# Kernel tuning notes

Hardware: AMD Instinct MI355X
Metric: run time of the kernel (lower is better)

The kernel has to match this reference:

```python
import jax, jax.numpy as jnp
import numpy as np

T, B, C, N, H = 4, 8, 256, 2048, 16
D = C // H          # head dim = 16
SCALE = 0.25        # fixed scale in SCA_AV
EPS = 1e-5          # BatchNorm eps


def _conv_bn(h_in, w, gamma, beta):
    """1x1 Conv1d (bias=False) + BatchNorm1d in training mode.
    h_in: [T,B,C,N]; w: [C_out,C_in]; BN stats over (T,B,N) per channel."""
    h = jnp.einsum('oc,tbcn->tbon', w, h_in)
    mean = h.mean(axis=(0, 1, 3), keepdims=True)
    var = ((h - mean) ** 2).mean(axis=(0, 1, 3), keepdims=True)
    return gamma[None, None, :, None] * (h - mean) * jax.lax.rsqrt(var + EPS) + beta[None, None, :, None]


def _spike(h, vth):
    # MyNode called once after reset: mem = 0/tau + h; spike = (mem >= vth)
    return (h >= vth).astype(h.dtype)


def _heads(z):
    # [T,B,C,N] -> [T,B,H,N,D] (channel index c = h*D + d, matching torch reshape)
    return z.reshape(T, B, H, D, N).transpose(0, 1, 2, 4, 3)


def setup_inputs() -> dict:
    key = jax.random.key(0)
    ks = jax.random.split(key, 16)
    s = 1.0 / np.sqrt(C)
    inp = {
        'x': jax.random.normal(ks[0], (T, B, C, N), jnp.float32),
        'y': jax.random.normal(ks[1], (T, B, C, N), jnp.float32),
        'q_w': jax.random.normal(ks[2], (C, C), jnp.float32) * s,
        'q_gamma': jnp.ones((C,), jnp.float32),
        'q_beta': jnp.zeros((C,), jnp.float32),
        'k_w': jax.random.normal(ks[3], (C, C), jnp.float32) * s,
        'k_gamma': jnp.ones((C,), jnp.float32),
        'k_beta': jnp.zeros((C,), jnp.float32),
        'v_w': jax.random.normal(ks[4], (C, C), jnp.float32) * s,
        'v_gamma': jnp.ones((C,), jnp.float32),
        'v_beta': jnp.zeros((C,), jnp.float32),
        'proj_w': jax.random.normal(ks[5], (C, C), jnp.float32) * s,
        'proj_gamma': jnp.ones((C,), jnp.float32),
        'proj_beta': jnp.zeros((C,), jnp.float32),
    }
    return inp


def reference(x, y, q_w, q_gamma, q_beta, k_w, k_gamma, k_beta,
              v_w, v_gamma, v_beta, proj_w, proj_gamma, proj_beta):
    # spiking Q from x, spiking K/V from y
    q = _heads(_spike(_conv_bn(x, q_w, q_gamma, q_beta), 1.0))  # [T,B,H,N,D] in {0,1}
    k = _heads(_spike(_conv_bn(y, k_w, k_gamma, k_beta), 1.0))
    v = _heads(_spike(_conv_bn(y, v_w, v_gamma, v_beta), 1.0))
    # linear-attention reordering: (q @ k^T) @ v == q @ (k^T @ v); kv is only DxD
    kv = jnp.einsum('tbhnd,tbhne->tbhde', k, v)          # [T,B,H,D,D]
    o = jnp.einsum('tbhnd,tbhde->tbhne', q, kv) * SCALE  # [T,B,H,N,D]
    # back to [T,B,C,N] (transpose(3,4) then reshape, as in torch)
    o = o.transpose(0, 1, 2, 4, 3).reshape(T, B, C, N)
    s = _spike(o, 0.5)                                   # attn_lif, v_threshold=0.5
    out = _spike(_conv_bn(s, proj_w, proj_gamma, proj_beta), 1.0)  # proj + proj_lif
    return out
```

## Files before the change

### kernel.cpp

```cpp
#include <hip/hip_runtime.h>
#include <stdint.h>
#include <math.h>

#define T_ 4
#define B_ 8
#define C_ 256
#define N_ 2048
#define TB_ 32
#define H_ 16
#define D_ 16
#define NTOT 65536
#define EPS 1e-5
#define NSLOT 1024
#define WPSZ 327680

typedef int v4i __attribute__((ext_vector_type(4)));

__global__ __launch_bounds__(256) void wprep_kernel(const float* __restrict__ W0,
                                                    const float* __restrict__ W1,
                                                    const float* __restrict__ W2,
                                                    int8_t* __restrict__ out) {
  const float* Wm = (blockIdx.y == 0) ? W0 : ((blockIdx.y == 1) ? W1 : W2);
  const int o = blockIdx.x;
  const int c = (int)threadIdx.x;
  double rr = rint((double)Wm[o * C_ + c] * 0x1p40);
  int8_t* base = out + (size_t)blockIdx.y * WPSZ + (size_t)(c >> 4) * 20480 +
                 (size_t)o * 80 + (c & 15);
#pragma unroll
  for (int L = 0; L < 5; ++L) {
    const double q = floor(fma(rr, 0.00390625, 0.5));
    const double d = fma(q, -256.0, rr);
    base[L * 16] = (int8_t)(int)d;
    rr = q;
  }
}

__global__ __launch_bounds__(256) void xprep_kernel(const float* __restrict__ X,
                                                    uint8_t* __restrict__ XP) {
  __shared__ float Xs[64][81];
  const int n0 = blockIdx.x * 64;
  const int tb = blockIdx.y;
  const int tid = (int)threadIdx.x;
  const int c_l = tid >> 2, nc = tid & 3;
  const int n_l = tid & 63, cq = tid >> 6;

  const float* Xp = X + ((size_t)(tb * C_ + c_l)) * N_ + n0 + nc * 16;

  for (int slab = 0; slab < 4; ++slab) {
    __syncthreads();
#pragma unroll
    for (int r = 0; r < 4; ++r) {
      const float4 xv = *(const float4*)(Xp + (size_t)(slab * 64) * N_ + 4 * r);
      Xs[c_l][nc * 16 + 4 * r + 0] = xv.x;
      Xs[c_l][nc * 16 + 4 * r + 1] = xv.y;
      Xs[c_l][nc * 16 + 4 * r + 2] = xv.z;
      Xs[c_l][nc * 16 + 4 * r + 3] = xv.w;
    }
    __syncthreads();
    uint32_t pk[4][4] = {};
#pragma unroll
    for (int s = 0; s < 16; ++s) {
      const float f = Xs[cq * 16 + s][n_l];
      union { double d; unsigned long long u; } cv;
      cv.d = fma((double)f, 0x1p28, 0x1.8p52);
      int v = (int)(uint32_t)(cv.u & 0xffffffffULL);
      const int d0 = (int)(int8_t)v;  v = (v - d0) >> 8;
      const int d1 = (int)(int8_t)v;  v = (v - d1) >> 8;
      const int d2 = (int)(int8_t)v;
      const int d3 = (v - d2) >> 8;
      const int sh = 8 * (s & 3);
      const int w = s >> 2;
      pk[0][w] |= (uint32_t)(d0 & 255) << sh;
      pk[1][w] |= (uint32_t)(d1 & 255) << sh;
      pk[2][w] |= (uint32_t)(d2 & 255) << sh;
      pk[3][w] |= (uint32_t)(d3 & 255) << sh;
    }
    uint8_t* dst =
        XP + (((size_t)(tb * 16 + slab * 4 + cq)) * (size_t)N_ + n0 + n_l) * 64;
#pragma unroll
    for (int j = 0; j < 4; ++j) {
      const int4 wv = make_int4((int)pk[j][0], (int)pk[j][1], (int)pk[j][2], (int)pk[j][3]);
      *(int4*)(dst + 16 * j) = wv;
    }
  }
}

template <bool QKV, bool STATS, typename OutT>
__global__ __launch_bounds__(256) void conv_i8(
    const int8_t* __restrict__ WP, const uint8_t* __restrict__ BP,
    double* __restrict__ Psum, double* __restrict__ Psq,
    const float* __restrict__ gamma, const float* __restrict__ beta,
    const double* __restrict__ mean, const double* __restrict__ invstd,
    OutT* __restrict__ Out) {
  __shared__ double dsum[4][64];
  __shared__ double dsq[4][64];
  __shared__ double aS[64];
  __shared__ double bS[64];
  const int n0 = blockIdx.x * 64;
  const int o0 = blockIdx.y * 64;
  const int tb = blockIdx.z;
  const int tid = (int)threadIdx.x;
  const int wv = tid >> 6;
  const int lane = tid & 63;
  const int l15 = lane & 15;
  const int g = lane >> 4;
  const int nn = 16 * wv + l15;

  if constexpr (!STATS) {
    if (tid < 64) {
      const int c = o0 + tid;
      const double is = invstd[c], mu = mean[c];
      const double gm = (double)gamma[c], bt = (double)beta[c];
      aS[tid] = gm * is;
      bS[tid] = bt - gm * mu * is;
    }
    __syncthreads();
  }

  v4i acc[4][5] = {};

  for (int slab = 0; slab < 4; ++slab) {
    const int cc = slab * 4 + g;
    v4i Bf[4];
    if constexpr (QKV) {
      const uint8_t* bp = BP + (((size_t)(tb * 16 + cc)) * (size_t)N_ + n0 + nn) * 64;
#pragma unroll
      for (int j = 0; j < 4; ++j) Bf[j] = *(const v4i*)(bp + 16 * j);
    } else {
      Bf[0] = *(const v4i*)(BP + ((size_t)(tb * N_ + n0 + nn)) * 256 + slab * 64 + 16 * g);
    }
#pragma unroll
    for (int mt = 0; mt < 4; ++mt) {
      const int8_t* ap = WP + (size_t)cc * 20480 + (size_t)(o0 + 16 * mt + l15) * 80;
      v4i A[5];
#pragma unroll
      for (int i = 0; i < 5; ++i) A[i] = *(const v4i*)(ap + 16 * i);
      if constexpr (QKV) {
        constexpr int PI[14] = {0, 1, 2, 3, 4, 1, 2, 3, 4, 2, 3, 4, 3, 4};
        constexpr int PJ[14] = {3, 3, 3, 3, 3, 2, 2, 2, 2, 1, 1, 1, 0, 0};
#pragma unroll
        for (int p = 0; p < 14; ++p)
          acc[mt][PI[p] + PJ[p] - 3] = __builtin_amdgcn_mfma_i32_16x16x64_i8(
              A[PI[p]], Bf[PJ[p]], acc[mt][PI[p] + PJ[p] - 3], 0, 0, 0);
      } else {
#pragma unroll
        for (int i = 0; i < 5; ++i)
          acc[mt][i] = __builtin_amdgcn_mfma_i32_16x16x64_i8(A[i], Bf[0], acc[mt][i], 0, 0, 0);
      }
    }
  }

  const double scale[5] = {QKV ? 0x1p-44 : 0x1p-40, QKV ? 0x1p-36 : 0x1p-32,
                           QKV ? 0x1p-28 : 0x1p-24, QKV ? 0x1p-20 : 0x1p-16,
                           QKV ? 0x1p-12 : 0x1p-8};

  if constexpr (STATS) {
#pragma unroll
    for (int mt = 0; mt < 4; ++mt) {
      double s[4], q[4];
#pragma unroll
      for (int r = 0; r < 4; ++r) {
        double v = 0.0;
#pragma unroll
        for (int a = 0; a < 5; ++a) v = fma(scale[a], (double)acc[mt][a][r], v);
        s[r] = v;
        q[r] = v * v;
      }
#pragma unroll
      for (int m = 1; m < 16; m <<= 1) {
#pragma unroll
        for (int r = 0; r < 4; ++r) {
          s[r] += __shfl_xor(s[r], m);
          q[r] += __shfl_xor(q[r], m);
        }
      }
      if (l15 < 4) {
        dsum[wv][16 * mt + 4 * g + l15] = s[l15];
        dsq[wv][16 * mt + 4 * g + l15] = q[l15];
      }
    }
    __syncthreads();
    if (tid < 64) {
      const double S = dsum[0][tid] + dsum[1][tid] + dsum[2][tid] + dsum[3][tid];
      const double Q = dsq[0][tid] + dsq[1][tid] + dsq[2][tid] + dsq[3][tid];
      const int slot = tb * 32 + (int)blockIdx.x;
      Psum[(size_t)(o0 + tid) * NSLOT + slot] = S;
      Psq[(size_t)(o0 + tid) * NSLOT + slot] = Q;
    }
  } else {
#pragma unroll
    for (int mt = 0; mt < 4; ++mt) {
#pragma unroll
      for (int r = 0; r < 4; ++r) {
        double v = 0.0;
#pragma unroll
        for (int a = 0; a < 5; ++a) v = fma(scale[a], (double)acc[mt][a][r], v);
        const int row = 16 * mt + 4 * g + r;
        const int sp = (aS[row] * v + bS[row] >= 1.0) ? 1 : 0;
        Out[((size_t)(tb * C_ + o0 + row)) * N_ + n0 + nn] = (OutT)sp;
      }
    }
  }
}

__global__ __launch_bounds__(256) void finalize_stats(const double* __restrict__ Psum,
                                                      const double* __restrict__ Psq,
                                                      double* __restrict__ mean,
                                                      double* __restrict__ invstd) {
  const int c = blockIdx.x;
  const int tid = (int)threadIdx.x;
  double s = 0.0, q = 0.0;
  for (int i = tid; i < NSLOT; i += 256) {
    s += Psum[(size_t)c * NSLOT + i];
    q += Psq[(size_t)c * NSLOT + i];
  }
#pragma unroll
  for (int m = 1; m < 64; m <<= 1) {
    s += __shfl_xor(s, m);
    q += __shfl_xor(q, m);
  }
  __shared__ double ls[4], lq[4];
  if ((tid & 63) == 0) {
    ls[tid >> 6] = s;
    lq[tid >> 6] = q;
  }
  __syncthreads();
  if (tid == 0) {
    const double S = ls[0] + ls[1] + ls[2] + ls[3];
    const double Q = lq[0] + lq[1] + lq[2] + lq[3];
    const double m = S / (double)NTOT;
    const double var = Q / (double)NTOT - m * m;
    mean[c] = m;
    invstd[c] = 1.0 / sqrt(var + EPS);
  }
}

__global__ __launch_bounds__(256) void attn_kernel(const uint8_t* __restrict__ Sq,
                                                   const uint8_t* __restrict__ Sk,
                                                   const uint8_t* __restrict__ Sv,
                                                   uint8_t* __restrict__ SbufT) {
  __shared__ float kvs[16][17];
  const int tb = (int)blockIdx.x >> 4;
  const int h = (int)blockIdx.x & 15;
  const size_t base = ((size_t)(tb * C_ + h * D_)) * N_;
  const int tid = (int)threadIdx.x;
  {
    const int d = tid >> 4, e = tid & 15;
    const uint32_t* kr = (const uint32_t*)(Sk + base + (size_t)d * N_);
    const uint32_t* vr = (const uint32_t*)(Sv + base + (size_t)e * N_);
    int cnt = 0;
    for (int i = 0; i < N_ / 4; ++i) cnt += __popc(kr[i] & vr[i]);
    kvs[d][e] = (float)cnt;
  }
  __syncthreads();
  for (int rep = 0; rep < 8; ++rep) {
    const int n = rep * 256 + tid;
    float qv[16];
#pragma unroll
    for (int d = 0; d < 16; ++d) qv[d] = (float)Sq[base + (size_t)d * N_ + n];
    uint32_t w[4] = {0, 0, 0, 0};
#pragma unroll
    for (int e = 0; e < 16; ++e) {
      float acc = 0.f;
#pragma unroll
      for (int d = 0; d < 16; ++d) acc += qv[d] * kvs[d][e];
      const uint32_t sp = (0.25f * acc >= 0.5f) ? 1u : 0u;
      w[e >> 2] |= sp << (8 * (e & 3));
    }
    const int4 pw = make_int4((int)w[0], (int)w[1], (int)w[2], (int)w[3]);
    *(int4*)(SbufT + ((size_t)(tb * N_ + n)) * 256 + h * 16) = pw;
  }
}

extern "C" void kernel_launch(void* const* d_in, const int* in_sizes, int n_in,
                              void* d_out, int out_size, void* d_ws, size_t ws_size,
                              hipStream_t stream) {
  const float* x   = (const float*)d_in[0];
  const float* y   = (const float*)d_in[1];
  const float* q_w = (const float*)d_in[2];
  const float* q_g = (const float*)d_in[3];
  const float* q_b = (const float*)d_in[4];
  const float* k_w = (const float*)d_in[5];
  const float* k_g = (const float*)d_in[6];
  const float* k_b = (const float*)d_in[7];
  const float* v_w = (const float*)d_in[8];
  const float* v_g = (const float*)d_in[9];
  const float* v_b = (const float*)d_in[10];
  const float* p_w = (const float*)d_in[11];
  const float* p_g = (const float*)d_in[12];
  const float* p_b = (const float*)d_in[13];
  float* out = (float*)d_out;

  char* ws = (char*)d_ws;
  const size_t NE = (size_t)TB_ * C_ * N_;
  uint8_t* XPx   = (uint8_t*)ws;
  uint8_t* XPy   = (uint8_t*)(ws + NE * 4);
  uint8_t* Sq    = (uint8_t*)(ws + NE * 8);
  uint8_t* Sk    = Sq + NE;
  uint8_t* Sv    = Sk + NE;
  uint8_t* SbufT = Sv + NE;

  double* PsumA   = (double*)SbufT;
  double* PsqA    = PsumA + (size_t)C_ * NSLOT;
  double* meanA   = PsqA + (size_t)C_ * NSLOT;
  double* invstdA = meanA + C_;
  int8_t* WPA     = (int8_t*)(SbufT + 5 * 1024 * 1024);
  int8_t* WPq     = WPA;
  int8_t* WPk     = WPA + WPSZ;
  int8_t* WPv     = WPA + 2 * WPSZ;
  double* PsumB   = (double*)Sq;
  double* PsqB    = PsumB + (size_t)C_ * NSLOT;
  double* meanB   = PsqB + (size_t)C_ * NSLOT;
  double* invstdB = meanB + C_;
  int8_t* WPB     = (int8_t*)(Sq + 8 * 1024 * 1024);

  const dim3 gridG(N_ / 64, C_ / 64, TB_);
  const dim3 blk(256);

  wprep_kernel<<<dim3(C_, 3), blk, 0, stream>>>(q_w, k_w, v_w, WPA);
  xprep_kernel<<<dim3(N_ / 64, TB_), blk, 0, stream>>>(x, XPx);
  xprep_kernel<<<dim3(N_ / 64, TB_), blk, 0, stream>>>(y, XPy);
  conv_i8<true, true, uint8_t><<<gridG, blk, 0, stream>>>(
      WPq, XPx, PsumA, PsqA, nullptr, nullptr, nullptr, nullptr, (uint8_t*)nullptr);
  finalize_stats<<<C_, blk, 0, stream>>>(PsumA, PsqA, meanA, invstdA);
  conv_i8<true, false, uint8_t><<<gridG, blk, 0, stream>>>(
      WPq, XPx, nullptr, nullptr, q_g, q_b, meanA, invstdA, Sq);
  conv_i8<true, true, uint8_t><<<gridG, blk, 0, stream>>>(
      WPk, XPy, PsumA, PsqA, nullptr, nullptr, nullptr, nullptr, (uint8_t*)nullptr);
  finalize_stats<<<C_, blk, 0, stream>>>(PsumA, PsqA, meanA, invstdA);
  conv_i8<true, false, uint8_t><<<gridG, blk, 0, stream>>>(
      WPk, XPy, nullptr, nullptr, k_g, k_b, meanA, invstdA, Sk);
  conv_i8<true, true, uint8_t><<<gridG, blk, 0, stream>>>(
      WPv, XPy, PsumA, PsqA, nullptr, nullptr, nullptr, nullptr, (uint8_t*)nullptr);
  finalize_stats<<<C_, blk, 0, stream>>>(PsumA, PsqA, meanA, invstdA);
  conv_i8<true, false, uint8_t><<<gridG, blk, 0, stream>>>(
      WPv, XPy, nullptr, nullptr, v_g, v_b, meanA, invstdA, Sv);
  attn_kernel<<<TB_ * H_, blk, 0, stream>>>(Sq, Sk, Sv, SbufT);
  wprep_kernel<<<dim3(C_, 1), blk, 0, stream>>>(p_w, p_w, p_w, WPB);
  conv_i8<false, true, float><<<gridG, blk, 0, stream>>>(
      WPB, SbufT, PsumB, PsqB, nullptr, nullptr, nullptr, nullptr, (float*)nullptr);
  finalize_stats<<<C_, blk, 0, stream>>>(PsumB, PsqB, meanB, invstdB);
  conv_i8<false, false, float><<<gridG, blk, 0, stream>>>(
      WPB, SbufT, nullptr, nullptr, p_g, p_b, meanB, invstdB, out);
}
```

Baseline: 821.9 us.

## Store conv output once and apply BN spike in separate elementwise pass

Each conv GEMM previously ran twice, once for BN statistics and once to apply BN and spike. Now it runs once, writes the pre-BN activations as a float plus an int8 residual (a split high-precision encoding) and accumulates stats, and a separate elementwise spike_pass applies the BN threshold. K and V spikes are bit-packed so the attention kv popcount reads eight times less data. The xprep buffer is reused for x and y. This trades a second MFMA GEMM for about 5 bytes per element of extra write-and-read traffic, and the residual encoding may lose precision near the threshold.

Result: faster. 677.2 us (-17.6%).

```diff
diff --git a/kernel.cpp b/kernel.cpp
--- a/kernel.cpp
+++ b/kernel.cpp
@@ -13,6 +13,7 @@
 #define EPS 1e-5
 #define NSLOT 1024
 #define WPSZ 327680
+#define MB (1024 * 1024)
 
 typedef int v4i __attribute__((ext_vector_type(4)));
 
@@ -85,17 +86,13 @@
   }
 }
 
-template <bool QKV, bool STATS, typename OutT>
-__global__ __launch_bounds__(256) void conv_i8(
+template <bool QKV>
+__global__ __launch_bounds__(256) void conv_gemm(
     const int8_t* __restrict__ WP, const uint8_t* __restrict__ BP,
-    double* __restrict__ Psum, double* __restrict__ Psq,
-    const float* __restrict__ gamma, const float* __restrict__ beta,
-    const double* __restrict__ mean, const double* __restrict__ invstd,
-    OutT* __restrict__ Out) {
+    float* __restrict__ hF, int8_t* __restrict__ hR,
+    double* __restrict__ Psum, double* __restrict__ Psq) {
   __shared__ double dsum[4][64];
   __shared__ double dsq[4][64];
-  __shared__ double aS[64];
-  __shared__ double bS[64];
   const int n0 = blockIdx.x * 64;
   const int o0 = blockIdx.y * 64;
   const int tb = blockIdx.z;
@@ -106,17 +103,6 @@
   const int g = lane >> 4;
   const int nn = 16 * wv + l15;
 
-  if constexpr (!STATS) {
-    if (tid < 64) {
-      const int c = o0 + tid;
-      const double is = invstd[c], mu = mean[c];
-      const double gm = (double)gamma[c], bt = (double)beta[c];
-      aS[tid] = gm * is;
-      bS[tid] = bt - gm * mu * is;
-    }
-    __syncthreads();
-  }
-
   v4i acc[4][5] = {};
 
   for (int slab = 0; slab < 4; ++slab) {
@@ -154,52 +140,44 @@
                            QKV ? 0x1p-28 : 0x1p-24, QKV ? 0x1p-20 : 0x1p-16,
                            QKV ? 0x1p-12 : 0x1p-8};
 
-  if constexpr (STATS) {
-#pragma unroll
-    for (int mt = 0; mt < 4; ++mt) {
-      double s[4], q[4];
+#pragma unroll
+  for (int mt = 0; mt < 4; ++mt) {
+    double s[4], q[4];
+#pragma unroll
+    for (int r = 0; r < 4; ++r) {
+      double v = 0.0;
+#pragma unroll
+      for (int a = 0; a < 5; ++a) v = fma(scale[a], (double)acc[mt][a][r], v);
+      const int row = 16 * mt + 4 * g + r;
+      const size_t idx = ((size_t)(tb * C_ + o0 + row)) * N_ + n0 + nn;
+      const float f = (float)v;
+      hF[idx] = f;
+      int ri = (int)rint((v - (double)f) * 0x1p27);
+      ri = ri < -127 ? -127 : (ri > 127 ? 127 : ri);
+      hR[idx] = (int8_t)ri;
+      s[r] = v;
+      q[r] = v * v;
+    }
+#pragma unroll
+    for (int m = 1; m < 16; m <<= 1) {
 #pragma unroll
       for (int r = 0; r < 4; ++r) {
-        double v = 0.0;
-#pragma unroll
-        for (int a = 0; a < 5; ++a) v = fma(scale[a], (double)acc[mt][a][r], v);
-        s[r] = v;
-        q[r] = v * v;
+        s[r] += __shfl_xor(s[r], m);
+        q[r] += __shfl_xor(q[r], m);
       }
-#pragma unroll
-      for (int m = 1; m < 16; m <<= 1) {
-#pragma unroll
-        for (int r = 0; r < 4; ++r) {
-          s[r] += __shfl_xor(s[r], m);
-          q[r] += __shfl_xor(q[r], m);
-        }
-      }
-      if (l15 < 4) {
-        dsum[wv][16 * mt + 4 * g + l15] = s[l15];
-        dsq[wv][16 * mt + 4 * g + l15] = q[l15];
-      }
-    }
-    __syncthreads();
-    if (tid < 64) {
-      const double S = dsum[0][tid] + dsum[1][tid] + dsum[2][tid] + dsum[3][tid];
-      const double Q = dsq[0][tid] + dsq[1][tid] + dsq[2][tid] + dsq[3][tid];
-      const int slot = tb * 32 + (int)blockIdx.x;
-      Psum[(size_t)(o0 + tid) * NSLOT + slot] = S;
-      Psq[(size_t)(o0 + tid) * NSLOT + slot] = Q;
-    }
-  } else {
-#pragma unroll
-    for (int mt = 0; mt < 4; ++mt) {
-#pragma unroll
-      for (int r = 0; r < 4; ++r) {
-        double v = 0.0;
-#pragma unroll
-        for (int a = 0; a < 5; ++a) v = fma(scale[a], (double)acc[mt][a][r], v);
-        const int row = 16 * mt + 4 * g + r;
-        const int sp = (aS[row] * v + bS[row] >= 1.0) ? 1 : 0;
-        Out[((size_t)(tb * C_ + o0 + row)) * N_ + n0 + nn] = (OutT)sp;
-      }
-    }
+    }
+    if (l15 < 4) {
+      dsum[wv][16 * mt + 4 * g + l15] = s[l15];
+      dsq[wv][16 * mt + 4 * g + l15] = q[l15];
+    }
+  }
+  __syncthreads();
+  if (tid < 64) {
+    const double S = dsum[0][tid] + dsum[1][tid] + dsum[2][tid] + dsum[3][tid];
+    const double Q = dsq[0][tid] + dsq[1][tid] + dsq[2][tid] + dsq[3][tid];
+    const int slot = tb * 32 + (int)blockIdx.x;
+    Psum[(size_t)(o0 + tid) * NSLOT + slot] = S;
+    Psq[(size_t)(o0 + tid) * NSLOT + slot] = Q;
   }
 }
 
@@ -235,21 +213,62 @@
   }
 }
 
-__global__ __launch_bounds__(256) void attn_kernel(const uint8_t* __restrict__ Sq,
-                                                   const uint8_t* __restrict__ Sk,
-                                                   const uint8_t* __restrict__ Sv,
+template <int MODE>
+__global__ __launch_bounds__(256) void spike_pass(
+    const float* __restrict__ hF, const int8_t* __restrict__ hR,
+    const float* __restrict__ gamma, const float* __restrict__ beta,
+    const double* __restrict__ mean, const double* __restrict__ invstd,
+    uint8_t* __restrict__ outB, float* __restrict__ outF) {
+  const size_t i0 = ((size_t)blockIdx.x * 256 + threadIdx.x) * 8;
+  const int c = (int)((i0 >> 11) & 255);
+  const double a = (double)gamma[c] * invstd[c];
+  const double b = (double)beta[c] - (double)gamma[c] * mean[c] * invstd[c];
+  const float4 f0 = *(const float4*)(hF + i0);
+  const float4 f1 = *(const float4*)(hF + i0 + 4);
+  const uint64_t rw = *(const uint64_t*)(hR + i0);
+  const float fs[8] = {f0.x, f0.y, f0.z, f0.w, f1.x, f1.y, f1.z, f1.w};
+  int sp[8];
+#pragma unroll
+  for (int j = 0; j < 8; ++j) {
+    const int8_t r8 = (int8_t)((rw >> (8 * j)) & 255);
+    const double v = (double)fs[j] + (double)r8 * 0x1p-27;
+    sp[j] = (a * v + b >= 1.0) ? 1 : 0;
+  }
+  if constexpr (MODE == 0) {
+    uint64_t w = 0;
+#pragma unroll
+    for (int j = 0; j < 8; ++j) w |= ((uint64_t)(uint8_t)sp[j]) << (8 * j);
+    *(uint64_t*)(outB + i0) = w;
+  } else if constexpr (MODE == 1) {
+    uint32_t byte = 0;
+#pragma unroll
+    for (int j = 0; j < 8; ++j) byte |= (uint32_t)sp[j] << j;
+    outB[i0 >> 3] = (uint8_t)byte;
+  } else {
+    *(float4*)(outF + i0) =
+        make_float4((float)sp[0], (float)sp[1], (float)sp[2], (float)sp[3]);
+    *(float4*)(outF + i0 + 4) =
+        make_float4((float)sp[4], (float)sp[5], (float)sp[6], (float)sp[7]);
+  }
+}
+
+__global__ __launch_bounds__(256) void attn_kernel(const uint8_t* __restrict__ SqB,
+                                                   const uint8_t* __restrict__ SkBit,
+                                                   const uint8_t* __restrict__ SvBit,
                                                    uint8_t* __restrict__ SbufT) {
   __shared__ float kvs[16][17];
   const int tb = (int)blockIdx.x >> 4;
   const int h = (int)blockIdx.x & 15;
-  const size_t base = ((size_t)(tb * C_ + h * D_)) * N_;
+  const size_t baseQ = ((size_t)(tb * C_ + h * D_)) * N_;
+  const size_t baseB = ((size_t)(tb * C_ + h * D_)) * (N_ / 8);
   const int tid = (int)threadIdx.x;
   {
     const int d = tid >> 4, e = tid & 15;
-    const uint32_t* kr = (const uint32_t*)(Sk + base + (size_t)d * N_);
-    const uint32_t* vr = (const uint32_t*)(Sv + base + (size_t)e * N_);
+    const uint32_t* kr = (const uint32_t*)(SkBit + baseB + (size_t)d * (N_ / 8));
+    const uint32_t* vr = (const uint32_t*)(SvBit + baseB + (size_t)e * (N_ / 8));
     int cnt = 0;
-    for (int i = 0; i < N_ / 4; ++i) cnt += __popc(kr[i] & vr[i]);
+#pragma unroll
+    for (int i = 0; i < N_ / 32; ++i) cnt += __popc(kr[i] & vr[i]);
     kvs[d][e] = (float)cnt;
   }
   __syncthreads();
@@ -257,7 +276,7 @@
     const int n = rep * 256 + tid;
     float qv[16];
 #pragma unroll
-    for (int d = 0; d < 16; ++d) qv[d] = (float)Sq[base + (size_t)d * N_ + n];
+    for (int d = 0; d < 16; ++d) qv[d] = (float)SqB[baseQ + (size_t)d * N_ + n];
     uint32_t w[4] = {0, 0, 0, 0};
 #pragma unroll
     for (int e = 0; e < 16; ++e) {
@@ -292,54 +311,42 @@
   float* out = (float*)d_out;
 
   char* ws = (char*)d_ws;
-  const size_t NE = (size_t)TB_ * C_ * N_;
-  uint8_t* XPx   = (uint8_t*)ws;
-  uint8_t* XPy   = (uint8_t*)(ws + NE * 4);
-  uint8_t* Sq    = (uint8_t*)(ws + NE * 8);
-  uint8_t* Sk    = Sq + NE;
-  uint8_t* Sv    = Sk + NE;
-  uint8_t* SbufT = Sv + NE;
-
-  double* PsumA   = (double*)SbufT;
-  double* PsqA    = PsumA + (size_t)C_ * NSLOT;
-  double* meanA   = PsqA + (size_t)C_ * NSLOT;
-  double* invstdA = meanA + C_;
-  int8_t* WPA     = (int8_t*)(SbufT + 5 * 1024 * 1024);
-  int8_t* WPq     = WPA;
-  int8_t* WPk     = WPA + WPSZ;
-  int8_t* WPv     = WPA + 2 * WPSZ;
-  double* PsumB   = (double*)Sq;
-  double* PsqB    = PsumB + (size_t)C_ * NSLOT;
-  double* meanB   = PsqB + (size_t)C_ * NSLOT;
-  double* invstdB = meanB + C_;
-  int8_t* WPB     = (int8_t*)(Sq + 8 * 1024 * 1024);
+  uint8_t* XP    = (uint8_t*)ws;
+  float*   hF    = (float*)(ws + (size_t)64 * MB);
+  int8_t*  hR    = (int8_t*)(ws + (size_t)128 * MB);
+  uint8_t* SqB   = (uint8_t*)(ws + (size_t)144 * MB);
+  uint8_t* SkBit = (uint8_t*)(ws + (size_t)160 * MB);
+  uint8_t* SvBit = (uint8_t*)(ws + (size_t)162 * MB);
+  uint8_t* SbufT = (uint8_t*)(ws + (size_t)164 * MB);
+  double*  Psum  = (double*)(ws + (size_t)180 * MB);
+  double*  Psq   = Psum + (size_t)C_ * NSLOT;
+  double*  mean   = (double*)(ws + (size_t)184 * MB);
+  double*  invstd = mean + C_;
+  int8_t*  WPA   = (int8_t*)(ws + (size_t)185 * MB);
+  int8_t*  WPq   = WPA;
+  int8_t*  WPk   = WPA + WPSZ;
+  int8_t*  WPv   = WPA + 2 * WPSZ;
+  int8_t*  WPB   = WPA + 3 * WPSZ;
 
   const dim3 gridG(N_ / 64, C_ / 64, TB_);
   const dim3 blk(256);
+  const int spikeBlocks = (int)((size_t)TB_ * C_ * N_ / (256 * 8));
 
   wprep_kernel<<<dim3(C_, 3), blk, 0, stream>>>(q_w, k_w, v_w, WPA);
-  xprep_kernel<<<dim3(N_ / 64, TB_), blk, 0, stream>>>(x, XPx);
-  xprep_kernel<<<dim3(N_ / 64, TB_), blk, 0, stream>>>(y, XPy);
-  conv_i8<true, true, uint8_t><<<gridG, blk, 0, stream>>>(
-      WPq, XPx, PsumA, PsqA, nullptr, nullptr, nullptr, nullptr, (uint8_t*)nullptr);
-  finalize_stats<<<C_, blk, 0, stream>>>(PsumA, PsqA, meanA, invstdA);
-  conv_i8<true, false, uint8_t><<<gridG, blk, 0, stream>>>(
-      WPq, XPx, nullptr, nullptr, q_g, q_b, meanA, invstdA, Sq);
-  conv_i8<true, true, uint8_t><<<gridG, blk, 0, stream>>>(
-      WPk, XPy, PsumA, PsqA, nullptr, nullptr, nullptr, nullptr, (uint8_t*)nullptr);
-  finalize_stats<<<C_, blk, 0, stream>>>(PsumA, PsqA, meanA, invstdA);
-  conv_i8<true, false, uint8_t><<<gridG, blk, 0, stream>>>(
-      WPk, XPy, nullptr, nullptr, k_g, k_b, meanA, invstdA, Sk);
-  conv_i8<true, true, uint8_t><<<gridG, blk, 0, stream>>>(
-      WPv, XPy, PsumA, PsqA, nullptr, nullptr, nullptr, nullptr, (uint8_t*)nullptr);
-  finalize_stats<<<C_, blk, 0, stream>>>(PsumA, PsqA, meanA, invstdA);
-  conv_i8<true, false, uint8_t><<<gridG, blk, 0, stream>>>(
-      WPv, XPy, nullptr, nullptr, v_g, v_b, meanA, invstdA, Sv);
-  attn_kernel<<<TB_ * H_, blk, 0, stream>>>(Sq, Sk, Sv, SbufT);
   wprep_kernel<<<dim3(C_, 1), blk, 0, stream>>>(p_w, p_w, p_w, WPB);
-  conv_i8<false, true, float><<<gridG, blk, 0, stream>>>(
-      WPB, SbufT, PsumB, PsqB, nullptr, nullptr, nullptr, nullptr, (float*)nullptr);
-  finalize_stats<<<C_, blk, 0, stream>>>(PsumB, PsqB, meanB, invstdB);
-  conv_i8<false, false, float><<<gridG, blk, 0, stream>>>(
-      WPB, SbufT, nullptr, nullptr, p_g, p_b, meanB, invstdB, out);
-}
+  xprep_kernel<<<dim3(N_ / 64, TB_), blk, 0, stream>>>(x, XP);
+  conv_gemm<true><<<gridG, blk, 0, stream>>>(WPq, XP, hF, hR, Psum, Psq);
+  finalize_stats<<<C_, blk, 0, stream>>>(Psum, Psq, mean, invstd);
+  spike_pass<0><<<spikeBlocks, blk, 0, stream>>>(hF, hR, q_g, q_b, mean, invstd, SqB, nullptr);
+  xprep_kernel<<<dim3(N_ / 64, TB_), blk, 0, stream>>>(y, XP);
+  conv_gemm<true><<<gridG, blk, 0, stream>>>(WPk, XP, hF, hR, Psum, Psq);
+  finalize_stats<<<C_, blk, 0, stream>>>(Psum, Psq, mean, invstd);
+  spike_pass<1><<<spikeBlocks, blk, 0, stream>>>(hF, hR, k_g, k_b, mean, invstd, SkBit, nullptr);
+  conv_gemm<true><<<gridG, blk, 0, stream>>>(WPv, XP, hF, hR, Psum, Psq);
+  finalize_stats<<<C_, blk, 0, stream>>>(Psum, Psq, mean, invstd);
+  spike_pass<1><<<spikeBlocks, blk, 0, stream>>>(hF, hR, v_g, v_b, mean, invstd, SvBit, nullptr);
+  attn_kernel<<<TB_ * H_, blk, 0, stream>>>(SqB, SkBit, SvBit, SbufT);
+  conv_gemm<false><<<gridG, blk, 0, stream>>>(WPB, SbufT, hF, hR, Psum, Psq);
+  finalize_stats<<<C_, blk, 0, stream>>>(Psum, Psq, mean, invstd);
+  spike_pass<2><<<spikeBlocks, blk, 0, stream>>>(hF, hR, p_g, p_b, mean, invstd, nullptr, out);
+}
```
